# Performance work log

Measured on AMD Instinct MI355X. Metric: run time of the kernel, lower is better.

Reference implementation:

```python
import jax, jax.numpy as jnp
import numpy as np

B, C, N, K, O = 8, 64, 4096, 20, 64
EPS = 1e-5


def setup_inputs() -> dict:
    key = jax.random.key(0)
    k1, k2, k3 = jax.random.split(key, 3)
    x = jax.random.normal(k1, (B, C, N), dtype=jnp.float32)
    # Conv2d(2C, O, kernel_size=1) -> weight [O, 2C], bias [O]
    fan_in = 2 * C
    bound = 1.0 / np.sqrt(fan_in)
    W = jax.random.uniform(k2, (O, 2 * C), minval=-bound, maxval=bound, dtype=jnp.float32)
    b = jax.random.uniform(k3, (O,), minval=-bound, maxval=bound, dtype=jnp.float32)
    gamma = jnp.ones((O,), dtype=jnp.float32)
    beta = jnp.zeros((O,), dtype=jnp.float32)
    return {"x": x, "W": W, "b": b, "gamma": gamma, "beta": beta}


def reference(x, W, b, gamma, beta):
    k = K
    Bs, Cs, Ns = x.shape
    x_t = jnp.transpose(x, (0, 2, 1))  # [B, N, C]
    # pairwise squared distances (monotonic with cdist, same topk indices)
    sq = jnp.sum(x_t * x_t, axis=-1)  # [B, N]
    d2 = sq[:, :, None] + sq[:, None, :] - 2.0 * jnp.einsum("bnc,bmc->bnm", x_t, x_t)
    valid_k = min(k, Ns - 1)
    _, idx = jax.lax.top_k(-d2, valid_k + 1)  # smallest distances
    idx = idx[:, :, 1:]  # drop self -> [B, N, k]
    # gather neighbor features per batch
    nbr = jax.vmap(lambda xt, i: xt[i])(x_t, idx)  # [B, N, k, C]
    central = x_t[:, :, None, :]  # [B, N, 1, C]
    edge = jnp.concatenate(
        [jnp.broadcast_to(central, (Bs, Ns, k, Cs)), nbr - central], axis=-1
    )  # [B, N, k, 2C]
    # 1x1 conv == channel matmul
    y = jnp.einsum("bnkc,oc->bonk", edge, W) + b[None, :, None, None]  # [B, O, N, k]
    # BatchNorm2d in training mode: batch statistics over (B, N, k)
    mean = jnp.mean(y, axis=(0, 2, 3), keepdims=True)
    var = jnp.var(y, axis=(0, 2, 3), keepdims=True)
    yn = (y - mean) * jax.lax.rsqrt(var + EPS)
    yn = gamma[None, :, None, None] * yn + beta[None, :, None, None]
    out = jax.nn.relu(yn)
    return jnp.max(out, axis=-1)  # [B, O, N]
```

## Files before the change

### kernel.cpp

```cpp
#include <hip/hip_runtime.h>
#include <hip/hip_bf16.h>

#define BB 8
#define CC 64
#define NN 4096
#define KK 20
#define OO 64
#define FMAXV 3.402823466e38f

typedef __attribute__((ext_vector_type(8))) short short8;
typedef __attribute__((ext_vector_type(4))) float f32x4;

__global__ __launch_bounds__(256) void kprep(const float* __restrict__ x,
                                             const float* __restrict__ W,
                                             const float* __restrict__ bias,
                                             float* __restrict__ xt,
                                             unsigned short* __restrict__ xb,
                                             float* __restrict__ sq,
                                             float* __restrict__ u,
                                             float* __restrict__ v) {
  __shared__ float tile[64][65];
  const int b = blockIdx.y, n0 = blockIdx.x * 64;
  const int lane = threadIdx.x & 63, grp = threadIdx.x >> 6;
  #pragma unroll
  for (int j = 0; j < 16; ++j) {
    int c = grp + j * 4;
    tile[c][lane] = x[((size_t)b * CC + c) * NN + n0 + lane];
  }
  float w2r[64], wdr[64];
  const float4* W4 = (const float4*)W;
  #pragma unroll
  for (int c4 = 0; c4 < 16; ++c4) {
    float4 q1 = W4[lane * 32 + c4];
    float4 q2 = W4[lane * 32 + 16 + c4];
    w2r[c4*4]=q2.x; w2r[c4*4+1]=q2.y; w2r[c4*4+2]=q2.z; w2r[c4*4+3]=q2.w;
    wdr[c4*4]=q1.x-q2.x; wdr[c4*4+1]=q1.y-q2.y; wdr[c4*4+2]=q1.z-q2.z; wdr[c4*4+3]=q1.w-q2.w;
  }
  const float bo = bias[lane];
  __syncthreads();
  #pragma unroll
  for (int j = 0; j < 16; ++j) {
    int n = grp + j * 4;
    float vv = tile[lane][n];
    size_t off = ((size_t)b * NN + n0 + n) * CC + lane;
    xt[off] = vv;
    unsigned int uu = __builtin_bit_cast(unsigned int, vv);
    xb[off] = (unsigned short)((uu + 0x7FFFu + ((uu >> 16) & 1u)) >> 16);
  }
  if (threadIdx.x < 64) {
    float s = 0.f;
    #pragma unroll
    for (int c = 0; c < 64; ++c) { float vv = tile[c][lane]; s += vv * vv; }
    sq[(size_t)b * NN + n0 + lane] = s;
  }
  for (int j = 0; j < 16; ++j) {
    int nl = grp * 16 + j;
    float du = 0.f, dv = 0.f;
    #pragma unroll
    for (int c = 0; c < 64; ++c) {
      float xv = tile[c][nl];
      du += w2r[c] * xv;
      dv += wdr[c] * xv;
    }
    size_t off = ((size_t)b * NN + n0 + nl) * OO + lane;
    u[off] = du;
    v[off] = dv + bo;
  }
}

__device__ __forceinline__ int lanes_below(unsigned long long m) {
  unsigned lo = (unsigned)m, hi = (unsigned)(m >> 32);
  int c = __builtin_amdgcn_mbcnt_lo(lo, 0);
  return (int)__builtin_amdgcn_mbcnt_hi(hi, (unsigned)c);
}

__device__ __forceinline__ unsigned packkey(float d, int m) {
  unsigned u = __builtin_bit_cast(unsigned, d);
  u ^= ((int)u < 0) ? 0xFFFFFFFFu : 0x80000000u;
  return (u & 0xFFFFF000u) | (unsigned)m;
}

__device__ __forceinline__ float unpackkey(unsigned t) {
  unsigned u = t | 0xFFFu;
  u = (u & 0x80000000u) ? (u ^ 0x80000000u) : ~u;
  return __builtin_bit_cast(float, u);
}

__device__ __forceinline__ unsigned bitonic64(unsigned v, int lane) {
  #pragma unroll
  for (int k = 2; k <= 64; k <<= 1) {
    #pragma unroll
    for (int j = k >> 1; j >= 1; j >>= 1) {
      unsigned o = (unsigned)__shfl_xor((int)v, j);
      bool up    = ((lane & k) == 0);
      bool lower = ((lane & j) == 0);
      unsigned mn = (v < o) ? v : o;
      unsigned mx = (v < o) ? o : v;
      v = (up == lower) ? mn : mx;
    }
  }
  return v;
}

__global__ __launch_bounds__(256, 4) void kknn7(const unsigned short* __restrict__ xb,
                                                const float* __restrict__ sq,
                                                unsigned* __restrict__ kcand) {
  __shared__ unsigned slist[4][16][32];
  __shared__ unsigned sbuf[4][16][128];
  const int lane = threadIdx.x & 63, w = threadIdx.x >> 6;
  const int wid = blockIdx.x * 4 + w;
  const int b = wid >> 9;
  const int half = (wid >> 8) & 1;
  const int n0g = (wid & 255) * 16;
  const int ch0 = half * (NN / 2);
  const int l15 = lane & 15, q = lane >> 4;
  const unsigned long long qmask = 0xFFFFull << (q * 16);

  const unsigned short* xbB = xb + (size_t)b * NN * CC;
  const float* sqB = sq + (size_t)b * NN;

  #pragma unroll
  for (int i = 0; i < 8; ++i) {
    int idx = i * 64 + lane;
    slist[w][idx >> 5][idx & 31] = 0xFFFFFFFFu;
  }

  short8 afr[2];
  #pragma unroll
  for (int ks = 0; ks < 2; ++ks)
    afr[ks] = __builtin_bit_cast(short8, *(const int4*)(xbB + (size_t)(n0g + l15) * CC + ks * 32 + q * 8));

  float tauf4[4];
  int cnt4[4], done4[4];
  #pragma unroll
  for (int j = 0; j < 4; ++j) { tauf4[j] = FMAXV; cnt4[j] = 0; done4[j] = 0; }

  for (int t = 0; t < 32; ++t) {
    const int cb = ch0 + t * 64;
    short8 bfr[4][2];
    float sv[4];
    #pragma unroll
    for (int ct = 0; ct < 4; ++ct) {
      #pragma unroll
      for (int ks = 0; ks < 2; ++ks)
        bfr[ct][ks] = __builtin_bit_cast(short8,
            *(const int4*)(xbB + (size_t)(cb + ct * 16 + l15) * CC + ks * 32 + q * 8));
      sv[ct] = sqB[cb + ct * 16 + l15];
    }
    f32x4 acc[4];
    #pragma unroll
    for (int ct = 0; ct < 4; ++ct) {
      acc[ct] = (f32x4){0.f, 0.f, 0.f, 0.f};
      acc[ct] = __builtin_amdgcn_mfma_f32_16x16x32_bf16(afr[0], bfr[ct][0], acc[ct], 0, 0, 0);
      acc[ct] = __builtin_amdgcn_mfma_f32_16x16x32_bf16(afr[1], bfr[ct][1], acc[ct], 0, 0, 0);
    }

    #pragma unroll
    for (int j = 0; j < 4; ++j) {
      float dv[4];
      bool  pj[4];
      #pragma unroll
      for (int ct = 0; ct < 4; ++ct) {
        dv[ct] = sv[ct] - 2.f * acc[ct][j];
        pj[ct] = dv[ct] <= tauf4[j];
      }
      unsigned long long b0 = __ballot(pj[0]);
      unsigned long long b1 = __ballot(pj[1]);
      unsigned long long b2 = __ballot(pj[2]);
      unsigned long long b3 = __ballot(pj[3]);
      if (!(b0 | b1 | b2 | b3)) continue;

      const int rowl = q * 4 + j;
      int base = cnt4[j];
      {
        unsigned long long bq = b0 & qmask;
        if (pj[0]) sbuf[w][rowl][(base + lanes_below(bq)) & 127] = packkey(dv[0], cb + 0 * 16 + l15);
        base += __popcll(bq);
      }
      {
        unsigned long long bq = b1 & qmask;
        if (pj[1]) sbuf[w][rowl][(base + lanes_below(bq)) & 127] = packkey(dv[1], cb + 1 * 16 + l15);
        base += __popcll(bq);
      }
      {
        unsigned long long bq = b2 & qmask;
        if (pj[2]) sbuf[w][rowl][(base + lanes_below(bq)) & 127] = packkey(dv[2], cb + 2 * 16 + l15);
        base += __popcll(bq);
      }
      {
        unsigned long long bq = b3 & qmask;
        if (pj[3]) sbuf[w][rowl][(base + lanes_below(bq)) & 127] = packkey(dv[3], cb + 3 * 16 + l15);
        base += __popcll(bq);
      }
      cnt4[j] = base;

      for (;;) {
        unsigned long long mb = __ballot(cnt4[j] - done4[j] >= 32);
        if (!mb) break;
        do {
          int src = __ffsll(mb) - 1;
          int qm = src >> 4;
          int rowm = qm * 4 + j;
          int dsrc = __shfl(done4[j], src);
          unsigned v = (lane < 32) ? slist[w][rowm][lane]
                                   : sbuf[w][rowm][(dsrc + lane - 32) & 127];
          v = bitonic64(v, lane);
          if (lane < 32) slist[w][rowm][lane] = v;
          unsigned tn = (unsigned)__shfl((int)v, 31);
          if (q == qm) { tauf4[j] = unpackkey(tn); done4[j] += 32; }
          mb &= ~(0xFFFFull << (qm * 16));
        } while (mb);
      }
    }
  }

  #pragma unroll
  for (int j = 0; j < 4; ++j) {
    unsigned long long mb = __ballot(cnt4[j] > done4[j]);
    while (mb) {
      int src = __ffsll(mb) - 1;
      int qm = src >> 4;
      int rowm = qm * 4 + j;
      int dsrc = __shfl(done4[j], src);
      int csrc = __shfl(cnt4[j], src);
      int rem = csrc - dsrc;
      unsigned v = (lane < 32) ? slist[w][rowm][lane]
                 : ((lane - 32) < rem ? sbuf[w][rowm][(dsrc + lane - 32) & 127] : 0xFFFFFFFFu);
      v = bitonic64(v, lane);
      if (lane < 32) slist[w][rowm][lane] = v;
      if (q == qm) done4[j] = cnt4[j];
      mb &= ~(0xFFFFull << (qm * 16));
    }
  }

  unsigned* kc = kcand + (((size_t)b * 2 + half) * NN + n0g) * 32;
  #pragma unroll
  for (int i = 0; i < 8; ++i) {
    int idx = i * 64 + lane;
    kc[idx] = slist[w][idx >> 5][idx & 31];
  }
}

__global__ __launch_bounds__(256) void kpost(const unsigned* __restrict__ kcand,
                                             const float* __restrict__ xt,
                                             const float* __restrict__ sq,
                                             const float* __restrict__ u,
                                             const float* __restrict__ v,
                                             float* __restrict__ umax,
                                             float* __restrict__ umin,
                                             float* __restrict__ gS) {
  const int lane = threadIdx.x & 63, w = threadIdx.x >> 6;
  const int gw = blockIdx.x * 4 + w;
  const int hl = lane & 31;
  float s1 = 0.f, s2 = 0.f;

  for (int it = 0; it < 2; ++it) {
    const int rbase = gw * 4 + it * 2;
    const int b = rbase >> 12;
    const int n = rbase & (NN - 1);

    const unsigned* kc0 = kcand + (((size_t)b * 2 + 0) * NN) * 32;
    const unsigned* kc1 = kcand + (((size_t)b * 2 + 1) * NN) * 32;
    unsigned vA = (lane < 32) ? kc0[(size_t)n * 32 + lane] : kc1[(size_t)n * 32 + (lane - 32)];
    vA = bitonic64(vA, lane);
    unsigned vB = (lane < 32) ? kc0[(size_t)(n + 1) * 32 + lane] : kc1[(size_t)(n + 1) * 32 + (lane - 32)];
    vB = bitonic64(vB, lane);
    unsigned kx = (unsigned)__shfl_xor((int)vB, 32);
    unsigned key = (lane < 32) ? vA : kx;
    int m = (int)(key & 0xFFFu);
    const int rowg = n + ((lane >= 32) ? 1 : 0);

    const float* xtB = xt + (size_t)b * NN * CC;
    const float* sqB = sq + (size_t)b * NN;
    const float4* pr = (const float4*)(xtB + (size_t)rowg * CC);
    const float4* pm = (const float4*)(xtB + (size_t)m * CC);
    float t0 = 0.f, t1 = 0.f, t2 = 0.f, t3 = 0.f;
    #pragma unroll
    for (int i = 0; i < 16; ++i) {
      float4 a = pr[i], c = pm[i];
      t0 += a.x * c.x; t1 += a.y * c.y; t2 += a.z * c.z; t3 += a.w * c.w;
    }
    float ev = sqB[m] - 2.f * ((t0 + t1) + (t2 + t3));

    #pragma unroll
    for (int k = 2; k <= 32; k <<= 1) {
      #pragma unroll
      for (int jj = k >> 1; jj >= 1; jj >>= 1) {
        float e2 = __shfl_xor(ev, jj);
        int   m2 = __shfl_xor(m, jj);
        bool up    = ((hl & k) == 0);
        bool lower = ((hl & jj) == 0);
        bool less  = (e2 < ev) || (e2 == ev && m2 < m);
        bool take  = (up == lower) ? less : !less;
        if (take) { ev = e2; m = m2; }
      }
    }

    const float* uB = u + (size_t)b * NN * OO;
    #pragma unroll
    for (int rr = 0; rr < 2; ++rr) {
      const int rown = n + rr;
      float vv = v[((size_t)b * NN + rown) * OO + lane];
      float mx = -FMAXV, mn = FMAXV;
      #pragma unroll
      for (int k = 0; k < KK; ++k) {
        int id = __shfl(m, rr * 32 + 1 + k);
        float uu = uB[(size_t)id * OO + lane];
        float y = vv + uu;
        s1 += y; s2 += y * y;
        mx = fmaxf(mx, uu); mn = fminf(mn, uu);
      }
      umax[((size_t)b * NN + rown) * OO + lane] = mx;
      umin[((size_t)b * NN + rown) * OO + lane] = mn;
    }
  }

  __shared__ float r1[4][64], r2[4][64];
  r1[w][lane] = s1; r2[w][lane] = s2;
  __syncthreads();
  if (w == 0) {
    float a = r1[0][lane] + r1[1][lane] + r1[2][lane] + r1[3][lane];
    float c = r2[0][lane] + r2[1][lane] + r2[2][lane] + r2[3][lane];
    float* g = gS + (blockIdx.x & 7) * 128;
    atomicAdd(&g[lane], a);
    atomicAdd(&g[64 + lane], c);
  }
}

__global__ __launch_bounds__(256) void kout(const float* __restrict__ v,
                                            const float* __restrict__ umax,
                                            const float* __restrict__ umin,
                                            const float* __restrict__ gS,
                                            const float* __restrict__ gamma,
                                            const float* __restrict__ beta,
                                            float* __restrict__ out) {
  __shared__ float sA[64], sB[64];
  __shared__ float zt[64][65];
  const int b = blockIdx.y, n0 = blockIdx.x * 64;
  const int lane = threadIdx.x & 63, w = threadIdx.x >> 6;
  if (threadIdx.x < 64) {
    float s1 = 0.f, s2 = 0.f;
    #pragma unroll
    for (int rsub = 0; rsub < 8; ++rsub) {
      s1 += gS[rsub * 128 + lane];
      s2 += gS[rsub * 128 + 64 + lane];
    }
    const float cnt = (float)BB * NN * KK;
    float m  = s1 / cnt;
    float var = s2 / cnt - m * m;
    float A = gamma[lane] * rsqrtf(var + 1e-5f);
    sA[lane] = A;
    sB[lane] = beta[lane] - A * m;
  }
  __syncthreads();
  for (int j = 0; j < 16; ++j) {
    int nl = w * 16 + j;
    size_t off = ((size_t)b * NN + n0 + nl) * OO + lane;
    float A = sA[lane];
    float c0 = A * v[off] + sB[lane];
    float z = c0 + A * ((A > 0.f) ? umax[off] : umin[off]);
    zt[nl][lane] = fmaxf(z, 0.f);
  }
  __syncthreads();
  for (int j = 0; j < 16; ++j) {
    int o = w * 16 + j;
    out[((size_t)b * OO + o) * NN + n0 + lane] = zt[lane][o];
  }
}

extern "C" void kernel_launch(void* const* d_in, const int* in_sizes, int n_in,
                              void* d_out, int out_size, void* d_ws, size_t ws_size,
                              hipStream_t stream) {
  const float* x     = (const float*)d_in[0];
  const float* W     = (const float*)d_in[1];
  const float* bias  = (const float*)d_in[2];
  const float* gamma = (const float*)d_in[3];
  const float* beta  = (const float*)d_in[4];
  float* out = (float*)d_out;

  float* xt  = (float*)d_ws;
  float* sq  = xt  + (size_t)BB*NN*CC;
  float* u   = sq  + (size_t)BB*NN;
  float* v   = u   + (size_t)BB*NN*OO;
  float* umx = v   + (size_t)BB*NN*OO;
  float* umn = umx + (size_t)BB*NN*OO;
  float* gS  = umn + (size_t)BB*NN*OO;
  unsigned short* xb = (unsigned short*)(gS + 1024);
  unsigned* kcand = (unsigned*)(xb + (size_t)BB*NN*CC);

  hipMemsetAsync(gS, 0, 1024 * sizeof(float), stream);
  kprep<<<dim3(NN/64, BB), 256, 0, stream>>>(x, W, bias, xt, xb, sq, u, v);
  kknn7<<<dim3(1024),      256, 0, stream>>>(xb, sq, kcand);
  kpost<<<dim3(2048),      256, 0, stream>>>(kcand, xt, sq, u, v, umx, umn, gS);
  kout <<<dim3(NN/64, BB), 256, 0, stream>>>(v, umx, umn, gS, gamma, beta, out);
}
```

Before: 404.5 us.

## Pair candidate-list merges per wave and seed lists from first tile

The KNN kernel now seeds each row's top-32 list by fully sorting the first 64 candidates instead of initializing to sentinels, so tau becomes tight right away and fewer candidates pass the filter. Pending merges are processed two rows at a time: each half-wave sorts 32 buffered candidates, which are reversed and combined with the existing sorted list through a single bitonic merge stage instead of a full 64-wide bitonic sort. This cuts shuffle and compare work in the selection phase at the cost of more complex control flow and extra shuffles for the reversal.

```diff
diff --git a/kernel.cpp b/kernel.cpp
--- a/kernel.cpp
+++ b/kernel.cpp
@@ -102,9 +102,83 @@
   return v;
 }
 
-__global__ __launch_bounds__(256, 4) void kknn7(const unsigned short* __restrict__ xb,
-                                                const float* __restrict__ sq,
-                                                unsigned* __restrict__ kcand) {
+__device__ __forceinline__ unsigned merge6(unsigned v, int lane) {
+  #pragma unroll
+  for (int j = 32; j >= 1; j >>= 1) {
+    unsigned o = (unsigned)__shfl_xor((int)v, j);
+    unsigned mn = (v < o) ? v : o;
+    unsigned mx = (v < o) ? o : v;
+    v = ((lane & j) == 0) ? mn : mx;
+  }
+  return v;
+}
+
+__device__ __forceinline__ void do_merges(unsigned long long mb, int j, int lane, int q,
+                                          unsigned (*sl)[32], unsigned (*rg)[128],
+                                          float& tau, int& cnt, int& done) {
+  const int hl = lane & 31;
+  while (mb) {
+    int srcA = __ffsll(mb) - 1;
+    int qA = srcA >> 4;
+    mb &= ~(0xFFFFull << (qA * 16));
+    if (mb) {
+      int srcB = __ffsll(mb) - 1;
+      int qB = srcB >> 4;
+      mb &= ~(0xFFFFull << (qB * 16));
+      const int rA = qA * 4 + j, rB = qB * 4 + j;
+      int dA = __shfl(done, srcA);
+      int rmA = __shfl(cnt, srcA) - dA;
+      int dB = __shfl(done, srcB);
+      int rmB = __shfl(cnt, srcB) - dB;
+      int tkA = (rmA < 32) ? rmA : 32;
+      int tkB = (rmB < 32) ? rmB : 32;
+      unsigned vs;
+      if (lane < 32) vs = (hl < tkA) ? rg[rA][(dA + hl) & 127] : 0xFFFFFFFFu;
+      else           vs = (hl < tkB) ? rg[rB][(dB + hl) & 127] : 0xFFFFFFFFu;
+      #pragma unroll
+      for (int k = 2; k <= 32; k <<= 1) {
+        #pragma unroll
+        for (int jj = k >> 1; jj >= 1; jj >>= 1) {
+          unsigned o = (unsigned)__shfl_xor((int)vs, jj);
+          bool up    = ((hl & k) == 0);
+          bool lower = ((hl & jj) == 0);
+          unsigned mn = (vs < o) ? vs : o;
+          unsigned mx = (vs < o) ? o : vs;
+          vs = (up == lower) ? mn : mx;
+        }
+      }
+      unsigned revA = (unsigned)__shfl((int)vs, (63 - lane) & 63);
+      unsigned revB = (unsigned)__shfl((int)vs, (95 - lane) & 63);
+      unsigned slA = (lane < 32) ? sl[rA][lane] : 0u;
+      unsigned va = (lane < 32) ? slA : revA;
+      va = merge6(va, lane);
+      if (lane < 32) sl[rA][lane] = va;
+      unsigned tnA = (unsigned)__shfl((int)va, 31);
+      unsigned slB = (lane < 32) ? sl[rB][lane] : 0u;
+      unsigned vb = (lane < 32) ? slB : revB;
+      vb = merge6(vb, lane);
+      if (lane < 32) sl[rB][lane] = vb;
+      unsigned tnB = (unsigned)__shfl((int)vb, 31);
+      if (q == qA) { tau = unpackkey(tnA); done += tkA; }
+      if (q == qB) { tau = unpackkey(tnB); done += tkB; }
+    } else {
+      const int rM = qA * 4 + j;
+      int dM = __shfl(done, srcA);
+      int rm = __shfl(cnt, srcA) - dM;
+      int tk = (rm < 32) ? rm : 32;
+      unsigned v = (lane < 32) ? sl[rM][lane]
+                 : ((lane - 32) < tk ? rg[rM][(dM + lane - 32) & 127] : 0xFFFFFFFFu);
+      v = bitonic64(v, lane);
+      if (lane < 32) sl[rM][lane] = v;
+      unsigned tn = (unsigned)__shfl((int)v, 31);
+      if (q == qA) { tau = unpackkey(tn); done += tk; }
+    }
+  }
+}
+
+__global__ __launch_bounds__(256, 4) void kknn12(const unsigned short* __restrict__ xb,
+                                                 const float* __restrict__ sq,
+                                                 unsigned* __restrict__ kcand) {
   __shared__ unsigned slist[4][16][32];
   __shared__ unsigned sbuf[4][16][128];
   const int lane = threadIdx.x & 63, w = threadIdx.x >> 6;
@@ -119,12 +193,6 @@
   const unsigned short* xbB = xb + (size_t)b * NN * CC;
   const float* sqB = sq + (size_t)b * NN;
 
-  #pragma unroll
-  for (int i = 0; i < 8; ++i) {
-    int idx = i * 64 + lane;
-    slist[w][idx >> 5][idx & 31] = 0xFFFFFFFFu;
-  }
-
   short8 afr[2];
   #pragma unroll
   for (int ks = 0; ks < 2; ++ks)
@@ -135,7 +203,43 @@
   #pragma unroll
   for (int j = 0; j < 4; ++j) { tauf4[j] = FMAXV; cnt4[j] = 0; done4[j] = 0; }
 
-  for (int t = 0; t < 32; ++t) {
+  {
+    const int cb = ch0;
+    short8 bfr[4][2];
+    float sv[4];
+    #pragma unroll
+    for (int ct = 0; ct < 4; ++ct) {
+      #pragma unroll
+      for (int ks = 0; ks < 2; ++ks)
+        bfr[ct][ks] = __builtin_bit_cast(short8,
+            *(const int4*)(xbB + (size_t)(cb + ct * 16 + l15) * CC + ks * 32 + q * 8));
+      sv[ct] = sqB[cb + ct * 16 + l15];
+    }
+    f32x4 acc[4];
+    #pragma unroll
+    for (int ct = 0; ct < 4; ++ct) {
+      acc[ct] = (f32x4){0.f, 0.f, 0.f, 0.f};
+      acc[ct] = __builtin_amdgcn_mfma_f32_16x16x32_bf16(afr[0], bfr[ct][0], acc[ct], 0, 0, 0);
+      acc[ct] = __builtin_amdgcn_mfma_f32_16x16x32_bf16(afr[1], bfr[ct][1], acc[ct], 0, 0, 0);
+    }
+    #pragma unroll
+    for (int j = 0; j < 4; ++j) {
+      const int rowl = q * 4 + j;
+      #pragma unroll
+      for (int ct = 0; ct < 4; ++ct)
+        sbuf[w][rowl][ct * 16 + l15] = packkey(sv[ct] - 2.f * acc[ct][j], cb + ct * 16 + l15);
+    }
+    #pragma unroll
+    for (int rowm = 0; rowm < 16; ++rowm) {
+      unsigned v = sbuf[w][rowm][lane];
+      v = bitonic64(v, lane);
+      if (lane < 32) slist[w][rowm][lane] = v;
+      unsigned tn = (unsigned)__shfl((int)v, 31);
+      if (q == (rowm >> 2)) tauf4[rowm & 3] = unpackkey(tn);
+    }
+  }
+
+  for (int t = 1; t < 32; ++t) {
     const int cb = ch0 + t * 64;
     short8 bfr[4][2];
     float sv[4];
@@ -197,19 +301,7 @@
       for (;;) {
         unsigned long long mb = __ballot(cnt4[j] - done4[j] >= 32);
         if (!mb) break;
-        do {
-          int src = __ffsll(mb) - 1;
-          int qm = src >> 4;
-          int rowm = qm * 4 + j;
-          int dsrc = __shfl(done4[j], src);
-          unsigned v = (lane < 32) ? slist[w][rowm][lane]
-                                   : sbuf[w][rowm][(dsrc + lane - 32) & 127];
-          v = bitonic64(v, lane);
-          if (lane < 32) slist[w][rowm][lane] = v;
-          unsigned tn = (unsigned)__shfl((int)v, 31);
-          if (q == qm) { tauf4[j] = unpackkey(tn); done4[j] += 32; }
-          mb &= ~(0xFFFFull << (qm * 16));
-        } while (mb);
+        do_merges(mb, j, lane, q, slist[w], sbuf[w], tauf4[j], cnt4[j], done4[j]);
       }
     }
   }
@@ -217,20 +309,7 @@
   #pragma unroll
   for (int j = 0; j < 4; ++j) {
     unsigned long long mb = __ballot(cnt4[j] > done4[j]);
-    while (mb) {
-      int src = __ffsll(mb) - 1;
-      int qm = src >> 4;
-      int rowm = qm * 4 + j;
-      int dsrc = __shfl(done4[j], src);
-      int csrc = __shfl(cnt4[j], src);
-      int rem = csrc - dsrc;
-      unsigned v = (lane < 32) ? slist[w][rowm][lane]
-                 : ((lane - 32) < rem ? sbuf[w][rowm][(dsrc + lane - 32) & 127] : 0xFFFFFFFFu);
-      v = bitonic64(v, lane);
-      if (lane < 32) slist[w][rowm][lane] = v;
-      if (q == qm) done4[j] = cnt4[j];
-      mb &= ~(0xFFFFull << (qm * 16));
-    }
+    if (mb) do_merges(mb, j, lane, q, slist[w], sbuf[w], tauf4[j], cnt4[j], done4[j]);
   }
 
   unsigned* kc = kcand + (((size_t)b * 2 + half) * NN + n0g) * 32;
@@ -390,7 +469,7 @@
 
   hipMemsetAsync(gS, 0, 1024 * sizeof(float), stream);
   kprep<<<dim3(NN/64, BB), 256, 0, stream>>>(x, W, bias, xt, xb, sq, u, v);
-  kknn7<<<dim3(1024),      256, 0, stream>>>(xb, sq, kcand);
+  kknn12<<<dim3(1024),     256, 0, stream>>>(xb, sq, kcand);
   kpost<<<dim3(2048),      256, 0, stream>>>(kcand, xt, sq, u, v, umx, umn, gS);
   kout <<<dim3(NN/64, BB), 256, 0, stream>>>(v, umx, umn, gS, gamma, beta, out);
 }
```

Result: faster. 374.0 us (-7.5%).
